# Optimization experiments

Measured on AMD Instinct MI355X. Metric: run time of the kernel, lower is better.

## Reference

```python
import jax, jax.numpy as jnp
import numpy as np


def _apply_rope(x, rope):
    # x: (B, T, D); rope: (T, D//2, 2) broadcast over batch
    B, T, D = x.shape
    x_ = x.reshape(B, T, D // 2, 2)
    cos, sin = rope[..., 0], rope[..., 1]
    xr, xi = x_[..., 0], x_[..., 1]
    rotr = xr * cos - xi * sin
    roti = xr * sin + xi * cos
    return jnp.stack([rotr, roti], axis=-1).reshape(B, T, D)


def setup_inputs() -> dict:
    key = jax.random.key(0)
    k1, k2, k3, k4 = jax.random.split(key, 4)
    B, T, D, H = 2, 2048, 1024, 16
    x = jax.random.normal(k1, (B, T, D), dtype=jnp.float32)
    rope = jax.random.normal(k2, (T, D // 2, 2), dtype=jnp.float32)
    w_qkv = jax.random.normal(k3, (3 * D, D), dtype=jnp.float32) * (1.0 / np.sqrt(D))
    w_proj = jax.random.normal(k4, (D, D), dtype=jnp.float32) * (1.0 / np.sqrt(D))
    return {"x": x, "rope": rope, "w_qkv": w_qkv, "w_proj": w_proj}


def reference(x, rope, w_qkv, w_proj):
    B, T, D = x.shape
    H = 16
    dk = D // H
    qkv = jnp.einsum("btd,ed->bte", x, w_qkv)  # (B, T, 3D)
    q, k, v = jnp.split(qkv, 3, axis=-1)
    q = _apply_rope(q, rope)
    k = _apply_rope(k, rope)
    # split heads: (B, H, T, dk)
    q = q.reshape(B, T, H, dk).transpose(0, 2, 1, 3)
    k = k.reshape(B, T, H, dk).transpose(0, 2, 1, 3)
    v = v.reshape(B, T, H, dk).transpose(0, 2, 1, 3)
    att = jnp.einsum("bhqd,bhkd->bhqk", q, k) / jnp.sqrt(jnp.float32(dk)).astype(x.dtype)
    att = jax.nn.softmax(att, axis=-1)
    out = jnp.einsum("bhqk,bhkd->bhqd", att, v)
    out = out.transpose(0, 2, 1, 3).reshape(B, T, D)
    return jnp.einsum("btd,ed->bte", out, w_proj)
```

## Files before the change

### kernel.cpp

```cpp
#include <hip/hip_runtime.h>

typedef _Float16 f16;
typedef _Float16 f16x2 __attribute__((ext_vector_type(2)));
typedef _Float16 f16x4 __attribute__((ext_vector_type(4)));
typedef _Float16 f16x8 __attribute__((ext_vector_type(8)));
typedef float    f32x2 __attribute__((ext_vector_type(2)));
typedef float    f32x4 __attribute__((ext_vector_type(4)));
typedef short    s16x4 __attribute__((ext_vector_type(4)));
typedef short    s16x8 __attribute__((ext_vector_type(8)));

#define GLDS16(gptr, lptr)                                                     \
  __builtin_amdgcn_global_load_lds(                                            \
      (const __attribute__((address_space(1))) void*)(gptr),                   \
      (__attribute__((address_space(3))) void*)(lptr), 16, 0, 0)

#define S_BARRIER() __builtin_amdgcn_s_barrier()
#define FENCE() asm volatile("" ::: "memory")
#define WAIT_VM8() asm volatile("s_waitcnt vmcnt(8)" ::: "memory")
#define WAIT_VM0() asm volatile("s_waitcnt vmcnt(0)" ::: "memory")
#define WAIT_LGKM0() asm volatile("s_waitcnt lgkmcnt(0)" ::: "memory")

__device__ inline short f32_to_bf16_rne(float f) {
  unsigned u = __builtin_bit_cast(unsigned, f);
  return (short)((u + 0x7FFFu + ((u >> 16) & 1u)) >> 16);
}

__global__ __launch_bounds__(256) void k_cast3(const float* __restrict__ a,
                                               const float* __restrict__ b,
                                               const float* __restrict__ c,
                                               f16* __restrict__ oa,
                                               f16* __restrict__ ob,
                                               f16* __restrict__ oc) {
  int i = blockIdx.x * 256 + threadIdx.x;
  const float* src;
  f16* dst;
  int off;
  if (i < 1048576) { src = a; dst = oa; off = i; }
  else if (i < 1835008) { src = b; dst = ob; off = i - 1048576; }
  else { src = c; dst = oc; off = i - 1835008; }
  f32x4 v = ((const f32x4*)src)[off];
  f16x4 h;
  h[0] = (f16)v[0]; h[1] = (f16)v[1]; h[2] = (f16)v[2]; h[3] = (f16)v[3];
  ((f16x4*)dst)[off] = h;
}

__global__ __launch_bounds__(256, 4) void k_gemm_qkv(
    const f16* __restrict__ A, const f16* __restrict__ B,
    const float* __restrict__ rope, f16* __restrict__ qh,
    f16* __restrict__ kh, short* __restrict__ vt) {
  const int K = 1024;
  __shared__ f16 sA[128 * 64];
  __shared__ f16 sB[128 * 64];
  const int tid = threadIdx.x;
  const int wave = tid >> 6, lane = tid & 63;
  const int lr = lane & 15, lq = lane >> 4;
  const int lr7 = lr & 7;
  const int wm = (wave >> 1) * 64, wn = (wave & 1) * 64;
  const size_t m0 = (size_t)blockIdx.x * 128, n0 = (size_t)blockIdx.y * 128;

  f32x4 acc[4][4] = {};

  const int sw8 = ((tid & 7) ^ ((tid >> 3) & 7)) * 8;
  const f16* ga = A + (m0 + (tid >> 3)) * (size_t)K + sw8;
  const f16* gb = B + (n0 + (tid >> 3)) * (size_t)K + sw8;

  for (int k0 = 0; k0 < K; k0 += 64) {
    __syncthreads();
#pragma unroll
    for (int r = 0; r < 4; ++r) {
      GLDS16(ga + (size_t)(r * 32) * K + k0, (char*)sA + r * 4096 + wave * 1024);
      GLDS16(gb + (size_t)(r * 32) * K + k0, (char*)sB + r * 4096 + wave * 1024);
    }
    __syncthreads();

#pragma unroll
    for (int kk = 0; kk < 2; ++kk) {
      f16x8 af[4], bf[4];
#pragma unroll
      for (int i = 0; i < 4; ++i)
        af[i] = *(const f16x8*)&sA[(wm + i * 16 + lr) * 64 +
                                   (((kk * 4 + lq) ^ lr7) * 8)];
#pragma unroll
      for (int j = 0; j < 4; ++j)
        bf[j] = *(const f16x8*)&sB[(wn + j * 16 + lr) * 64 +
                                   (((kk * 4 + lq) ^ lr7) * 8)];
#pragma unroll
      for (int i = 0; i < 4; ++i)
#pragma unroll
        for (int j = 0; j < 4; ++j)
          acc[i][j] = __builtin_amdgcn_mfma_f32_16x16x32_f16(af[i], bf[j],
                                                             acc[i][j], 0, 0, 0);
    }
  }

  const int region = (int)(n0 >> 10);
  if (region == 2) {
#pragma unroll
    for (int i = 0; i < 4; ++i)
#pragma unroll
      for (int j = 0; j < 4; ++j) {
        int e = (int)(n0 + wn + j * 16 + lr) - 2048;
        int h = e >> 6, c = e & 63;
        int m = (int)(m0 + wm + i * 16 + lq * 4);
        int b = m >> 11, t0 = m & 2047;
        s16x4 o;
#pragma unroll
        for (int r = 0; r < 4; ++r) o[r] = f32_to_bf16_rne(acc[i][j][r]);
        *(s16x4*)&vt[(((size_t)(b * 16 + h)) * 64 + c) * 2048 + t0] = o;
      }
  } else {
    const float scl = region == 0 ? 0.1803368801111204f : 1.0f;
    f16* dst = region == 0 ? qh : kh;
    const int odd = lr & 1;
#pragma unroll
    for (int i = 0; i < 4; ++i)
#pragma unroll
      for (int j = 0; j < 4; ++j) {
        int e = ((int)(n0 + wn + j * 16 + lr)) & 1023;
        int h = e >> 6, c = e & 63, p = e >> 1;
        int mb = (int)(m0 + wm + i * 16 + lq * 4);
        int b = mb >> 11;
#pragma unroll
        for (int r = 0; r < 4; ++r) {
          int t = (mb + r) & 2047;
          float v = acc[i][j][r];
          float partner = __shfl_xor(v, 1);
          f32x2 cs = *(const f32x2*)&rope[((size_t)t * 512 + p) * 2];
          float out = odd ? (partner * cs[1] + v * cs[0])
                          : (v * cs[0] - partner * cs[1]);
          dst[(((size_t)(b * 16 + h)) * 2048 + t) * 64 + c] = (f16)(out * scl);
        }
      }
  }
}

__global__ __launch_bounds__(256, 4) void k_gemm_bt(const f16* __restrict__ A,
                                                    const f16* __restrict__ B,
                                                    float* __restrict__ C,
                                                    int M, int N, int K) {
  __shared__ f16 sA[128 * 64];
  __shared__ f16 sB[128 * 64];
  const int tid = threadIdx.x;
  const int wave = tid >> 6, lane = tid & 63;
  const int lr = lane & 15, lq = lane >> 4;
  const int lr7 = lr & 7;
  const int wm = (wave >> 1) * 64, wn = (wave & 1) * 64;
  const size_t m0 = (size_t)blockIdx.x * 128, n0 = (size_t)blockIdx.y * 128;

  f32x4 acc[4][4] = {};

  const int sw8 = ((tid & 7) ^ ((tid >> 3) & 7)) * 8;
  const f16* ga = A + (m0 + (tid >> 3)) * (size_t)K + sw8;
  const f16* gb = B + (n0 + (tid >> 3)) * (size_t)K + sw8;

  for (int k0 = 0; k0 < K; k0 += 64) {
    __syncthreads();
#pragma unroll
    for (int r = 0; r < 4; ++r) {
      GLDS16(ga + (size_t)(r * 32) * K + k0, (char*)sA + r * 4096 + wave * 1024);
      GLDS16(gb + (size_t)(r * 32) * K + k0, (char*)sB + r * 4096 + wave * 1024);
    }
    __syncthreads();

#pragma unroll
    for (int kk = 0; kk < 2; ++kk) {
      f16x8 af[4], bf[4];
#pragma unroll
      for (int i = 0; i < 4; ++i)
        af[i] = *(const f16x8*)&sA[(wm + i * 16 + lr) * 64 +
                                   (((kk * 4 + lq) ^ lr7) * 8)];
#pragma unroll
      for (int j = 0; j < 4; ++j)
        bf[j] = *(const f16x8*)&sB[(wn + j * 16 + lr) * 64 +
                                   (((kk * 4 + lq) ^ lr7) * 8)];
#pragma unroll
      for (int i = 0; i < 4; ++i)
#pragma unroll
        for (int j = 0; j < 4; ++j)
          acc[i][j] = __builtin_amdgcn_mfma_f32_16x16x32_f16(af[i], bf[j],
                                                             acc[i][j], 0, 0, 0);
    }
  }

#pragma unroll
  for (int i = 0; i < 4; ++i)
#pragma unroll
    for (int j = 0; j < 4; ++j)
#pragma unroll
      for (int r = 0; r < 4; ++r)
        C[(m0 + wm + i * 16 + lq * 4 + r) * (size_t)N + n0 + wn + j * 16 + lr] =
            acc[i][j][r];
}

__global__ __launch_bounds__(256, 2) void k_attn(const f16* __restrict__ Qp,
                                                 const f16* __restrict__ Kp,
                                                 const short* __restrict__ Vt,
                                                 f16* __restrict__ Op) {
  __shared__ f16 sQ[128 * 64];
  __shared__ f16 sKV[2 * 16384];
  const int tid = threadIdx.x, wave = tid >> 6, lane = tid & 63;
  const int lr = lane & 15, lq = lane >> 4;
  const int lr7 = lr & 7;
  const int bh = blockIdx.x, qt = blockIdx.y;
  const size_t base = (size_t)bh * 2048 * 64;

  const int sw8 = ((tid & 7) ^ ((tid >> 3) & 7)) * 8;
  const int sw16 = ((tid & 15) ^ ((tid >> 4) & 15)) * 8;

  const int rowlo = tid >> 3;
  const int pw = 8 * ((rowlo >> 2) & 3) + 4 * (rowlo >> 4) + (rowlo & 3);

  auto stage_kv = [&](int jcc, int d) {
    const f16* gk = Kp + base + (size_t)jcc * 128 * 64;
    const short* gv = Vt + base + (size_t)jcc * 128;
    char* bK = (char*)sKV + d * 32768;
    char* bV = bK + 16384;
#pragma unroll
    for (int r = 0; r < 4; ++r) {
      GLDS16(gk + (size_t)(r * 32 + pw) * 64 + sw8,
             bK + r * 4096 + wave * 1024);
      GLDS16(gv + (size_t)(r * 16 + (tid >> 4)) * 2048 + sw16,
             bV + r * 4096 + wave * 1024);
    }
  };

  const f16* gq = Qp + base + (size_t)qt * 128 * 64;
#pragma unroll
  for (int r = 0; r < 4; ++r)
    GLDS16(gq + (size_t)(r * 32 + rowlo) * 64 + sw8,
           (char*)sQ + r * 4096 + wave * 1024);
  stage_kv(0, 0);
  WAIT_VM8();
  S_BARRIER();
  FENCE();
  f16x8 qa0 = *(const f16x8*)&sQ[(wave * 32 + lr) * 64 + ((lq ^ lr7) * 8)];
  f16x8 qa1 = *(const f16x8*)&sQ[(wave * 32 + lr) * 64 + (((4 + lq) ^ lr7) * 8)];
  f16x8 qb0 = *(const f16x8*)&sQ[(wave * 32 + 16 + lr) * 64 + ((lq ^ lr7) * 8)];
  f16x8 qb1 =
      *(const f16x8*)&sQ[(wave * 32 + 16 + lr) * 64 + (((4 + lq) ^ lr7) * 8)];

  f32x4 ota[4] = {}, otb[4] = {};
  float la = 0.f, lb = 0.f;

#pragma unroll 1
  for (int jc = 0; jc < 16; ++jc) {
    const int cur = jc & 1;
    if (jc < 15) {
      stage_kv(jc + 1, cur ^ 1);
      WAIT_VM8();
    } else {
      WAIT_VM0();
    }
    S_BARRIER();
    FENCE();

    const f16* bK = (const f16*)((char*)sKV + cur * 32768);
    const short* bV = (const short*)((char*)sKV + cur * 32768 + 16384);

    s16x8 pfa8[4], pfb8[4];
#pragma unroll
    for (int nt = 0; nt < 8; ++nt) {
      f16x8 kf0 = *(const f16x8*)&bK[(nt * 16 + lr) * 64 + ((lq ^ lr7) * 8)];
      f16x8 kf1 =
          *(const f16x8*)&bK[(nt * 16 + lr) * 64 + (((4 + lq) ^ lr7) * 8)];
      f32x4 z = {0.f, 0.f, 0.f, 0.f};
      f32x4 sa = __builtin_amdgcn_mfma_f32_16x16x32_f16(kf0, qa0, z, 0, 0, 0);
      sa = __builtin_amdgcn_mfma_f32_16x16x32_f16(kf1, qa1, sa, 0, 0, 0);
      f32x4 sb = __builtin_amdgcn_mfma_f32_16x16x32_f16(kf0, qb0, z, 0, 0, 0);
      sb = __builtin_amdgcn_mfma_f32_16x16x32_f16(kf1, qb1, sb, 0, 0, 0);
#pragma unroll
      for (int r = 0; r < 4; ++r) {
        float pa = __builtin_amdgcn_exp2f(sa[r]);
        float pb = __builtin_amdgcn_exp2f(sb[r]);
        la += pa; lb += pb;
        pfa8[nt >> 1][(nt & 1) * 4 + r] =
            (short)(__builtin_bit_cast(unsigned, pa) >> 16);
        pfb8[nt >> 1][(nt & 1) * 4 + r] =
            (short)(__builtin_bit_cast(unsigned, pb) >> 16);
      }
    }

#pragma unroll
    for (int d = 0; d < 4; ++d)
#pragma unroll
      for (int g = 0; g < 4; ++g) {
        s16x8 vf =
            *(const s16x8*)&bV[(d * 16 + lr) * 128 + (((g * 4 + lq) ^ lr) * 8)];
        ota[d] = __builtin_amdgcn_mfma_f32_16x16x32_bf16(vf, pfa8[g], ota[d],
                                                         0, 0, 0);
        otb[d] = __builtin_amdgcn_mfma_f32_16x16x32_bf16(vf, pfb8[g], otb[d],
                                                         0, 0, 0);
      }

    WAIT_LGKM0();
    S_BARRIER();
    FENCE();
  }

  la += __shfl_xor(la, 16); la += __shfl_xor(la, 32);
  lb += __shfl_xor(lb, 16); lb += __shfl_xor(lb, 32);
  float rla = 1.f / la, rlb = 1.f / lb;
  int b = bh >> 4, h = bh & 15;
  int ta = qt * 128 + wave * 32 + lr;
  f16* gouta = Op + ((size_t)(b * 2048 + ta)) * 1024 + h * 64;
  f16* goutb = gouta + (size_t)16 * 1024;
#pragma unroll
  for (int d = 0; d < 4; ++d) {
    f16x4 oa, ob;
#pragma unroll
    for (int r = 0; r < 4; ++r) {
      oa[r] = (f16)(ota[d][r] * rla);
      ob[r] = (f16)(otb[d][r] * rlb);
    }
    *(f16x4*)&gouta[d * 16 + lq * 4] = oa;
    *(f16x4*)&goutb[d * 16 + lq * 4] = ob;
  }
}

extern "C" void kernel_launch(void* const* d_in, const int* in_sizes, int n_in,
                              void* d_out, int out_size, void* d_ws,
                              size_t ws_size, hipStream_t stream) {
  const float* x     = (const float*)d_in[0];
  const float* rope  = (const float*)d_in[1];
  const float* wqkv  = (const float*)d_in[2];
  const float* wproj = (const float*)d_in[3];
  float* out = (float*)d_out;

  char* w = (char*)d_ws;
  const size_t MB = 1024 * 1024;
  f16* xh   = (f16*)(w + 0);
  f16* wqh  = (f16*)(w + 8 * MB);
  f16* wph  = (f16*)(w + 14 * MB);
  f16* qh   = (f16*)(w + 16 * MB);
  f16* kh   = (f16*)(w + 24 * MB);
  short* vth = (short*)(w + 32 * MB);
  f16* aoh  = (f16*)(w + 40 * MB);

  k_cast3<<<8192, 256, 0, stream>>>(x, wqkv, wproj, xh, wqh, wph);

  k_gemm_qkv<<<dim3(32, 24), 256, 0, stream>>>(xh, wqh, rope, qh, kh, vth);

  k_attn<<<dim3(32, 16), 256, 0, stream>>>(qh, kh, vth, aoh);

  k_gemm_bt<<<dim3(32, 8), 256, 0, stream>>>(aoh, wph, out, 4096, 1024, 1024);
}
```

Baseline: 184.9 us.

## Double-buffer LDS tiles in QKV and projection GEMMs with BK=32 prefetch

```diff
diff --git a/kernel.cpp b/kernel.cpp
--- a/kernel.cpp
+++ b/kernel.cpp
@@ -17,6 +17,7 @@
 #define S_BARRIER() __builtin_amdgcn_s_barrier()
 #define FENCE() asm volatile("" ::: "memory")
 #define WAIT_VM8() asm volatile("s_waitcnt vmcnt(8)" ::: "memory")
+#define WAIT_VM4() asm volatile("s_waitcnt vmcnt(4)" ::: "memory")
 #define WAIT_VM0() asm volatile("s_waitcnt vmcnt(0)" ::: "memory")
 #define WAIT_LGKM0() asm volatile("s_waitcnt lgkmcnt(0)" ::: "memory")
 
@@ -49,48 +50,63 @@
     const float* __restrict__ rope, f16* __restrict__ qh,
     f16* __restrict__ kh, short* __restrict__ vt) {
   const int K = 1024;
-  __shared__ f16 sA[128 * 64];
-  __shared__ f16 sB[128 * 64];
+  __shared__ f16 sA[2][4096];
+  __shared__ f16 sB[2][4096];
   const int tid = threadIdx.x;
   const int wave = tid >> 6, lane = tid & 63;
   const int lr = lane & 15, lq = lane >> 4;
-  const int lr7 = lr & 7;
   const int wm = (wave >> 1) * 64, wn = (wave & 1) * 64;
   const size_t m0 = (size_t)blockIdx.x * 128, n0 = (size_t)blockIdx.y * 128;
 
   f32x4 acc[4][4] = {};
 
-  const int sw8 = ((tid & 7) ^ ((tid >> 3) & 7)) * 8;
-  const f16* ga = A + (m0 + (tid >> 3)) * (size_t)K + sw8;
-  const f16* gb = B + (n0 + (tid >> 3)) * (size_t)K + sw8;
-
-  for (int k0 = 0; k0 < K; k0 += 64) {
-    __syncthreads();
-#pragma unroll
-    for (int r = 0; r < 4; ++r) {
-      GLDS16(ga + (size_t)(r * 32) * K + k0, (char*)sA + r * 4096 + wave * 1024);
-      GLDS16(gb + (size_t)(r * 32) * K + k0, (char*)sB + r * 4096 + wave * 1024);
-    }
-    __syncthreads();
-
-#pragma unroll
-    for (int kk = 0; kk < 2; ++kk) {
-      f16x8 af[4], bf[4];
-#pragma unroll
-      for (int i = 0; i < 4; ++i)
-        af[i] = *(const f16x8*)&sA[(wm + i * 16 + lr) * 64 +
-                                   (((kk * 4 + lq) ^ lr7) * 8)];
+  const int gsw = ((tid & 3) ^ ((tid >> 3) & 3)) * 8;
+  const f16* ga = A + (m0 + (tid >> 2)) * (size_t)K + gsw;
+  const f16* gb = B + (n0 + (tid >> 2)) * (size_t)K + gsw;
+  const int swr = (lr >> 1) & 3;
+
+  auto stage = [&](int it, int d) {
+    const int k0 = it * 32;
+#pragma unroll
+    for (int r = 0; r < 2; ++r) {
+      GLDS16(ga + (size_t)(r * 64) * K + k0,
+             (char*)sA[d] + r * 4096 + wave * 1024);
+      GLDS16(gb + (size_t)(r * 64) * K + k0,
+             (char*)sB[d] + r * 4096 + wave * 1024);
+    }
+  };
+
+  stage(0, 0);
+#pragma unroll 1
+  for (int it = 0; it < 32; ++it) {
+    const int cur = it & 1;
+    if (it < 31) {
+      stage(it + 1, cur ^ 1);
+      WAIT_VM4();
+    } else {
+      WAIT_VM0();
+    }
+    S_BARRIER();
+    FENCE();
+
+    f16x8 af[4], bf[4];
+#pragma unroll
+    for (int i = 0; i < 4; ++i)
+      af[i] = *(const f16x8*)&sA[cur][(wm + i * 16 + lr) * 32 +
+                                      ((lq ^ swr) * 8)];
+#pragma unroll
+    for (int j = 0; j < 4; ++j)
+      bf[j] = *(const f16x8*)&sB[cur][(wn + j * 16 + lr) * 32 +
+                                      ((lq ^ swr) * 8)];
+#pragma unroll
+    for (int i = 0; i < 4; ++i)
 #pragma unroll
       for (int j = 0; j < 4; ++j)
-        bf[j] = *(const f16x8*)&sB[(wn + j * 16 + lr) * 64 +
-                                   (((kk * 4 + lq) ^ lr7) * 8)];
-#pragma unroll
-      for (int i = 0; i < 4; ++i)
-#pragma unroll
-        for (int j = 0; j < 4; ++j)
-          acc[i][j] = __builtin_amdgcn_mfma_f32_16x16x32_f16(af[i], bf[j],
-                                                             acc[i][j], 0, 0, 0);
-    }
+        acc[i][j] = __builtin_amdgcn_mfma_f32_16x16x32_f16(af[i], bf[j],
+                                                           acc[i][j], 0, 0, 0);
+    WAIT_LGKM0();
+    S_BARRIER();
+    FENCE();
   }
 
   const int region = (int)(n0 >> 10);
@@ -138,48 +154,64 @@
                                                     const f16* __restrict__ B,
                                                     float* __restrict__ C,
                                                     int M, int N, int K) {
-  __shared__ f16 sA[128 * 64];
-  __shared__ f16 sB[128 * 64];
+  __shared__ f16 sA[2][4096];
+  __shared__ f16 sB[2][4096];
   const int tid = threadIdx.x;
   const int wave = tid >> 6, lane = tid & 63;
   const int lr = lane & 15, lq = lane >> 4;
-  const int lr7 = lr & 7;
   const int wm = (wave >> 1) * 64, wn = (wave & 1) * 64;
   const size_t m0 = (size_t)blockIdx.x * 128, n0 = (size_t)blockIdx.y * 128;
 
   f32x4 acc[4][4] = {};
 
-  const int sw8 = ((tid & 7) ^ ((tid >> 3) & 7)) * 8;
-  const f16* ga = A + (m0 + (tid >> 3)) * (size_t)K + sw8;
-  const f16* gb = B + (n0 + (tid >> 3)) * (size_t)K + sw8;
-
-  for (int k0 = 0; k0 < K; k0 += 64) {
-    __syncthreads();
-#pragma unroll
-    for (int r = 0; r < 4; ++r) {
-      GLDS16(ga + (size_t)(r * 32) * K + k0, (char*)sA + r * 4096 + wave * 1024);
-      GLDS16(gb + (size_t)(r * 32) * K + k0, (char*)sB + r * 4096 + wave * 1024);
-    }
-    __syncthreads();
-
-#pragma unroll
-    for (int kk = 0; kk < 2; ++kk) {
-      f16x8 af[4], bf[4];
-#pragma unroll
-      for (int i = 0; i < 4; ++i)
-        af[i] = *(const f16x8*)&sA[(wm + i * 16 + lr) * 64 +
-                                   (((kk * 4 + lq) ^ lr7) * 8)];
+  const int gsw = ((tid & 3) ^ ((tid >> 3) & 3)) * 8;
+  const f16* ga = A + (m0 + (tid >> 2)) * (size_t)K + gsw;
+  const f16* gb = B + (n0 + (tid >> 2)) * (size_t)K + gsw;
+  const int swr = (lr >> 1) & 3;
+
+  auto stage = [&](int it, int d) {
+    const int k0 = it * 32;
+#pragma unroll
+    for (int r = 0; r < 2; ++r) {
+      GLDS16(ga + (size_t)(r * 64) * K + k0,
+             (char*)sA[d] + r * 4096 + wave * 1024);
+      GLDS16(gb + (size_t)(r * 64) * K + k0,
+             (char*)sB[d] + r * 4096 + wave * 1024);
+    }
+  };
+
+  const int iters = K >> 5;
+  stage(0, 0);
+#pragma unroll 1
+  for (int it = 0; it < iters; ++it) {
+    const int cur = it & 1;
+    if (it < iters - 1) {
+      stage(it + 1, cur ^ 1);
+      WAIT_VM4();
+    } else {
+      WAIT_VM0();
+    }
+    S_BARRIER();
+    FENCE();
+
+    f16x8 af[4], bf[4];
+#pragma unroll
+    for (int i = 0; i < 4; ++i)
+      af[i] = *(const f16x8*)&sA[cur][(wm + i * 16 + lr) * 32 +
+                                      ((lq ^ swr) * 8)];
+#pragma unroll
+    for (int j = 0; j < 4; ++j)
+      bf[j] = *(const f16x8*)&sB[cur][(wn + j * 16 + lr) * 32 +
+                                      ((lq ^ swr) * 8)];
+#pragma unroll
+    for (int i = 0; i < 4; ++i)
 #pragma unroll
       for (int j = 0; j < 4; ++j)
-        bf[j] = *(const f16x8*)&sB[(wn + j * 16 + lr) * 64 +
-                                   (((kk * 4 + lq) ^ lr7) * 8)];
-#pragma unroll
-      for (int i = 0; i < 4; ++i)
-#pragma unroll
-        for (int j = 0; j < 4; ++j)
-          acc[i][j] = __builtin_amdgcn_mfma_f32_16x16x32_f16(af[i], bf[j],
-                                                             acc[i][j], 0, 0, 0);
-    }
+        acc[i][j] = __builtin_amdgcn_mfma_f32_16x16x32_f16(af[i], bf[j],
+                                                           acc[i][j], 0, 0, 0);
+    WAIT_LGKM0();
+    S_BARRIER();
+    FENCE();
   }
 
 #pragma unroll
```

Result: no change. 185.6 us (+0.4%).
